# Kernel optimization log

Measured on AMD Instinct MI355X. Metric: run time of the kernel, lower is better.

The kernel has to match this reference:

```python
import jax, jax.numpy as jnp
import numpy as np

N_NODES = 100000
N_EDGES = 1600000
F_IN, F_HID, F_OUT = 128, 256, 128


def setup_inputs() -> dict:
    key = jax.random.key(0)
    ks = jax.random.split(key, 9)
    x = jax.random.normal(ks[0], (N_NODES, F_IN), dtype=jnp.float32)
    edge_src = jax.random.randint(ks[1], (N_EDGES,), 0, N_NODES, dtype=jnp.int32)
    edge_dst = jax.random.randint(ks[2], (N_EDGES,), 0, N_NODES, dtype=jnp.int32)
    s1 = 1.0 / np.sqrt(F_IN)
    s2 = 1.0 / np.sqrt(F_HID)
    W_self1 = jax.random.uniform(ks[3], (F_IN, F_HID), jnp.float32, -s1, s1)
    W_neigh1 = jax.random.uniform(ks[4], (F_IN, F_HID), jnp.float32, -s1, s1)
    b1 = jnp.zeros((F_HID,), jnp.float32)
    W_self2 = jax.random.uniform(ks[5], (F_HID, F_OUT), jnp.float32, -s2, s2)
    W_neigh2 = jax.random.uniform(ks[6], (F_HID, F_OUT), jnp.float32, -s2, s2)
    b2 = jnp.zeros((F_OUT,), jnp.float32)
    return {"x": x, "edge_src": edge_src, "edge_dst": edge_dst,
            "W_self1": W_self1, "W_neigh1": W_neigh1, "b1": b1,
            "W_self2": W_self2, "W_neigh2": W_neigh2, "b2": b2}


def _sage_mean(h, src, dst, W_self, W_neigh, b):
    # mean-aggregate neighbor features onto dst nodes (DGL SAGEConv 'mean')
    deg = jax.ops.segment_sum(jnp.ones_like(src, dtype=h.dtype), dst,
                              num_segments=N_NODES)
    neigh_sum = jax.ops.segment_sum(h[src], dst, num_segments=N_NODES)
    neigh = neigh_sum / jnp.maximum(deg, 1.0)[:, None]
    return h @ W_self + neigh @ W_neigh + b


def reference(x, edge_src, edge_dst, W_self1, W_neigh1, b1, W_self2, W_neigh2, b2):
    h = _sage_mean(x, edge_src, edge_dst, W_self1, W_neigh1, b1)
    h = jax.nn.sigmoid(h)
    h = _sage_mean(h, edge_src, edge_dst, W_self2, W_neigh2, b2)
    return h
```

## Files before the change

### kernel.cpp

```cpp
#include <hip/hip_runtime.h>
#include <hip/hip_bf16.h>

#define N_NODES 100000
#define N_EDGES 1600000
#define F_IN 128
#define F_HID 256
#define F_OUT 128

typedef unsigned short ushort_t;
typedef __attribute__((ext_vector_type(4))) float f32x4;
typedef __attribute__((ext_vector_type(8))) short bf16x8;

#define GAS __attribute__((address_space(1)))
#define LAS __attribute__((address_space(3)))

__device__ __forceinline__ float bf2f(ushort_t u) {
    unsigned int x = ((unsigned int)u) << 16;
    return __builtin_bit_cast(float, x);
}
__device__ __forceinline__ ushort_t f2bf(float f) {
    unsigned int x = __builtin_bit_cast(unsigned int, f);
    unsigned int r = (x + 0x7fffu + ((x >> 16) & 1u)) >> 16;
    return (ushort_t)r;
}

#define NBUCK ((N_NODES + 255) >> 8)
#define CHUNK 4096

__global__ __launch_bounds__(256) void bucket_count_kernel(
    const int* __restrict__ dst, int* __restrict__ bucket_cnt, int n) {
    __shared__ int hist[NBUCK];
    int tid = threadIdx.x;
    int e0 = blockIdx.x * CHUNK;
    int cnt = n - e0; if (cnt > CHUNK) cnt = CHUNK;
    for (int b = tid; b < NBUCK; b += 256) hist[b] = 0;
    __syncthreads();
    for (int i = tid; i < cnt; i += 256) {
        int d = __builtin_nontemporal_load(dst + e0 + i);
        atomicAdd(&hist[d >> 8], 1);
    }
    __syncthreads();
    for (int b = tid; b < NBUCK; b += 256)
        if (hist[b]) atomicAdd(&bucket_cnt[b], hist[b]);
}

__global__ __launch_bounds__(512) void bucket_scan_kernel(
    const int* __restrict__ bucket_cnt, int* __restrict__ bbase,
    int* __restrict__ bcursor, int* __restrict__ rowptr) {
    __shared__ int tmp[512];
    int tid = threadIdx.x;
    int v = (tid < NBUCK) ? bucket_cnt[tid] : 0;
    tmp[tid] = v;
    __syncthreads();
#pragma unroll
    for (int off = 1; off < 512; off <<= 1) {
        int t = (tid >= off) ? tmp[tid - off] : 0;
        __syncthreads();
        tmp[tid] += t;
        __syncthreads();
    }
    if (tid < NBUCK) {
        int base = tmp[tid] - v;
        bbase[tid] = base;
        bcursor[tid] = base;
    }
    if (tid == 0) {
        bbase[NBUCK] = N_EDGES;
        rowptr[N_NODES] = N_EDGES;
    }
}

__global__ __launch_bounds__(256) void bin_edges_kernel(
    const int* __restrict__ src, const int* __restrict__ dst,
    int* __restrict__ bcursor, unsigned int* __restrict__ pairs, int n) {
    __shared__ int sdst[CHUNK];
    __shared__ int ssrc[CHUNK];
    __shared__ int hist[NBUCK];
    __shared__ int resv[NBUCK];
    int tid = threadIdx.x;
    int e0 = blockIdx.x * CHUNK;
    int cnt = n - e0; if (cnt > CHUNK) cnt = CHUNK;
    for (int b = tid; b < NBUCK; b += 256) hist[b] = 0;
    __syncthreads();
    for (int i = tid; i < cnt; i += 256) {
        int d = __builtin_nontemporal_load(dst + e0 + i);
        int s = __builtin_nontemporal_load(src + e0 + i);
        sdst[i] = d;
        ssrc[i] = s;
        atomicAdd(&hist[d >> 8], 1);
    }
    __syncthreads();
    for (int b = tid; b < NBUCK; b += 256) {
        int h = hist[b];
        resv[b] = h ? atomicAdd(&bcursor[b], h) : 0;
        hist[b] = 0;
    }
    __syncthreads();
    for (int i = tid; i < cnt; i += 256) {
        int d = sdst[i], s = ssrc[i];
        int b = d >> 8;
        int off = atomicAdd(&hist[b], 1);
        pairs[resv[b] + off] = ((unsigned)(d & 255) << 17) | (unsigned)s;
    }
}

__global__ __launch_bounds__(256) void sort_bucket_kernel(
    const unsigned int* __restrict__ pairs, const int* __restrict__ bbase,
    int* __restrict__ rowptr, float* __restrict__ invdeg,
    int* __restrict__ csr_src, int nNodes) {
    __shared__ int lcnt[256];
    __shared__ int lrp[256];
    int tid = threadIdx.x;
    int base = blockIdx.x << 8;
    int nn = nNodes - base; if (nn > 256) nn = 256;
    lcnt[tid] = 0;
    __syncthreads();
    int e0 = bbase[blockIdx.x], e1 = bbase[blockIdx.x + 1];
    for (int i = e0 + tid; i < e1; i += 256)
        atomicAdd(&lcnt[pairs[i] >> 17], 1);
    __syncthreads();
    int v = lcnt[tid];
    lrp[tid] = v;
    __syncthreads();
#pragma unroll
    for (int off = 1; off < 256; off <<= 1) {
        int t = (tid >= off) ? lrp[tid - off] : 0;
        __syncthreads();
        lrp[tid] += t;
        __syncthreads();
    }
    lcnt[tid] = 0;
    lrp[tid] = lrp[tid] - v + e0;
    if (tid < nn) {
        rowptr[base + tid] = lrp[tid];
        invdeg[base + tid] = 1.0f / fmaxf((float)v, 1.0f);
    }
    __syncthreads();
    for (int i = e0 + tid; i < e1; i += 256) {
        unsigned pv = pairs[i];
        int j = (int)(pv >> 17);
        int off = atomicAdd(&lcnt[j], 1);
        csr_src[lrp[j] + off] = (int)(pv & 0x1FFFFu);
    }
}

__global__ __launch_bounds__(256) void convert_x_kernel(const float* __restrict__ x,
                                                        ushort_t* __restrict__ A1, int n4) {
    int i = blockIdx.x * 256 + threadIdx.x;
    if (i >= n4) return;
    int e = i * 4;
    int row = e >> 7;
    int col = e & 127;
    f32x4 v = __builtin_nontemporal_load((const f32x4*)(x + (size_t)row * F_IN + col));
    ushort4 o;
    o.x = f2bf(v.x); o.y = f2bf(v.y); o.z = f2bf(v.z); o.w = f2bf(v.w);
    *(ushort4*)(A1 + (size_t)row * 256 + col) = o;
}

__global__ __launch_bounds__(256) void wtransK_kernel(const float* __restrict__ W1,
                                                      const float* __restrict__ W2,
                                                      ushort_t* __restrict__ Wt,
                                                      int Kx, int Ktot, int N) {
    int i = blockIdx.x * 256 + threadIdx.x;
    if (i >= N * Ktot) return;
    int n = i / Ktot, k = i - n * Ktot;
    float v = (k < Kx) ? W1[(size_t)k * N + n] : W2[(size_t)(k - Kx) * N + n];
    Wt[(size_t)n * Ktot + k] = f2bf(v);
}

__global__ __launch_bounds__(256) void wtransN_kernel(const float* __restrict__ Wa,
                                                      const float* __restrict__ Wb,
                                                      ushort_t* __restrict__ Wt,
                                                      int K, int Nh) {
    int i = blockIdx.x * 256 + threadIdx.x;
    if (i >= 2 * Nh * K) return;
    int n = i / K, k = i - n * K;
    const float* W = (n < Nh) ? Wa : Wb;
    int nn = (n < Nh) ? n : n - Nh;
    Wt[(size_t)n * K + k] = f2bf(W[(size_t)k * Nh + nn]);
}

#define ACC8(v)                                                     \
    acc[0] += bf2f((ushort_t)((v).x & 0xffffu));                    \
    acc[1] += bf2f((ushort_t)((v).x >> 16));                        \
    acc[2] += bf2f((ushort_t)((v).y & 0xffffu));                    \
    acc[3] += bf2f((ushort_t)((v).y >> 16));                        \
    acc[4] += bf2f((ushort_t)((v).z & 0xffffu));                    \
    acc[5] += bf2f((ushort_t)((v).z >> 16));                        \
    acc[6] += bf2f((ushort_t)((v).w & 0xffffu));                    \
    acc[7] += bf2f((ushort_t)((v).w >> 16));

template <int MODE>
__global__ __launch_bounds__(256) void gather16_kernel(
    const ushort_t* __restrict__ H, int ldh,
    const int* __restrict__ rowptr, const int* __restrict__ csr_src,
    const float* __restrict__ invdeg,
    const ushort_t* __restrict__ uself, int ldu,
    const float* __restrict__ bias,
    void* __restrict__ outp, int ldo, int nNodes) {
    int lane = threadIdx.x & 63;
    int node = blockIdx.x * 4 + (threadIdx.x >> 6);
    if (node >= nNodes) return;
    int grp = lane >> 4, sub = lane & 15;
    int start = rowptr[node], end = rowptr[node + 1];
    const size_t cofs = (size_t)sub * 8;
    float acc[8] = {};
    for (int e = start + grp; e < end; e += 16) {
        int s0 = csr_src[e];
        uint4 v0 = *(const uint4*)(H + (size_t)s0 * ldh + cofs);
        bool p1 = (e + 4) < end;
        int s1 = p1 ? csr_src[e + 4] : s0;
        uint4 v1 = *(const uint4*)(H + (size_t)s1 * ldh + cofs);
        bool p2 = (e + 8) < end;
        int s2 = p2 ? csr_src[e + 8] : s0;
        uint4 v2 = *(const uint4*)(H + (size_t)s2 * ldh + cofs);
        bool p3 = (e + 12) < end;
        int s3 = p3 ? csr_src[e + 12] : s0;
        uint4 v3 = *(const uint4*)(H + (size_t)s3 * ldh + cofs);
        ACC8(v0);
        if (p1) { ACC8(v1); }
        if (p2) { ACC8(v2); }
        if (p3) { ACC8(v3); }
    }
#pragma unroll
    for (int j = 0; j < 8; ++j) {
        acc[j] += __shfl_xor(acc[j], 16);
        acc[j] += __shfl_xor(acc[j], 32);
    }
    if (grp == 0) {
        float sc = invdeg[node];
        if (MODE == 0) {
            uint4 o;
            o.x = (unsigned)f2bf(acc[0] * sc) | ((unsigned)f2bf(acc[1] * sc) << 16);
            o.y = (unsigned)f2bf(acc[2] * sc) | ((unsigned)f2bf(acc[3] * sc) << 16);
            o.z = (unsigned)f2bf(acc[4] * sc) | ((unsigned)f2bf(acc[5] * sc) << 16);
            o.w = (unsigned)f2bf(acc[6] * sc) | ((unsigned)f2bf(acc[7] * sc) << 16);
            *(uint4*)((ushort_t*)outp + (size_t)node * ldo + cofs) = o;
        } else {
            uint4 us = *(const uint4*)(uself + (size_t)node * ldu + cofs);
            f32x4 o0, o1;
            o0.x = acc[0] * sc + bf2f((ushort_t)(us.x & 0xffffu)) + bias[cofs + 0];
            o0.y = acc[1] * sc + bf2f((ushort_t)(us.x >> 16)) + bias[cofs + 1];
            o0.z = acc[2] * sc + bf2f((ushort_t)(us.y & 0xffffu)) + bias[cofs + 2];
            o0.w = acc[3] * sc + bf2f((ushort_t)(us.y >> 16)) + bias[cofs + 3];
            o1.x = acc[4] * sc + bf2f((ushort_t)(us.z & 0xffffu)) + bias[cofs + 4];
            o1.y = acc[5] * sc + bf2f((ushort_t)(us.z >> 16)) + bias[cofs + 5];
            o1.z = acc[6] * sc + bf2f((ushort_t)(us.w & 0xffffu)) + bias[cofs + 6];
            o1.w = acc[7] * sc + bf2f((ushort_t)(us.w >> 16)) + bias[cofs + 7];
            float* op = (float*)outp + (size_t)node * ldo + cofs;
            __builtin_nontemporal_store(o0, (f32x4*)op);
            __builtin_nontemporal_store(o1, (f32x4*)(op + 4));
        }
    }
}

__global__ __launch_bounds__(256) void gemm_mfma_kernel(
    const ushort_t* __restrict__ A,
    const ushort_t* __restrict__ Bt,
    const float* __restrict__ bias,
    ushort_t* __restrict__ Cout,
    int M, int N, int K, int mode) {
    __shared__ ushort_t shmem[2 * 128 * 64];
    ushort_t* As = shmem;
    ushort_t* Bs = shmem + 128 * 64;
    int tid = threadIdx.x;
    int lane = tid & 63, wid = tid >> 6;
    int l15 = lane & 15, kgrp = lane >> 4, l7 = lane & 7, l8 = lane >> 3;
    int bm = blockIdx.x * 128, bn = blockIdx.y * 128;
    int wr = (wid >> 1) * 64, wc = (wid & 1) * 64;

    f32x4 acc[4][4] = {};

    for (int k0 = 0; k0 < K; k0 += 64) {
#pragma unroll
        for (int t = 0; t < 4; ++t) {
            int c = wid * 4 + t;
            int row = c * 8 + l8;
            int scol = ((l7 ^ (row & 7)) << 3);
            int ar = bm + row; if (ar > M - 1) ar = M - 1;
            __builtin_amdgcn_global_load_lds(
                (const GAS void*)(A + (size_t)ar * K + k0 + scol),
                (LAS void*)(&As[c * 512]), 16, 0, 0);
            int br = bn + row;
            __builtin_amdgcn_global_load_lds(
                (const GAS void*)(Bt + (size_t)br * K + k0 + scol),
                (LAS void*)(&Bs[c * 512]), 16, 0, 0);
        }
        __syncthreads();
#pragma unroll
        for (int kk = 0; kk < 2; ++kk) {
            bf16x8 af[4], bfv[4];
#pragma unroll
            for (int mi = 0; mi < 4; ++mi) {
                int row = wr + mi * 16 + l15;
                int kel = (kk * 32 + kgrp * 8) ^ ((row & 7) << 3);
                af[mi] = *(const bf16x8*)(&As[row * 64 + kel]);
            }
#pragma unroll
            for (int ni = 0; ni < 4; ++ni) {
                int row = wc + ni * 16 + l15;
                int kel = (kk * 32 + kgrp * 8) ^ ((row & 7) << 3);
                bfv[ni] = *(const bf16x8*)(&Bs[row * 64 + kel]);
            }
#pragma unroll
            for (int mi = 0; mi < 4; ++mi)
#pragma unroll
                for (int ni = 0; ni < 4; ++ni)
                    acc[mi][ni] = __builtin_amdgcn_mfma_f32_16x16x32_bf16(
                        af[mi], bfv[ni], acc[mi][ni], 0, 0, 0);
        }
        __syncthreads();
    }

    ushort_t* my = shmem + wid * 4096;
#pragma unroll
    for (int mi = 0; mi < 4; ++mi) {
#pragma unroll
        for (int ni = 0; ni < 4; ++ni) {
            int gcol = bn + wc + ni * 16 + l15;
#pragma unroll
            for (int r = 0; r < 4; ++r) {
                float v = acc[mi][ni][r];
                if (mode == 0) {
                    v += bias[gcol];
                    v = 1.0f / (1.0f + __expf(-v));
                }
                int lr = mi * 16 + kgrp * 4 + r;
                int lc = (ni * 16 + l15) ^ (kgrp << 3);
                my[lr * 64 + lc] = f2bf(v);
            }
        }
    }
#pragma unroll
    for (int it = 0; it < 8; ++it) {
        int r2 = (lane >> 3) + it * 8;
        int c2 = ((lane & 7) << 3) ^ (((r2 >> 2) & 3) << 3);
        bf16x8 vv = *(const bf16x8*)(&my[r2 * 64 + c2]);
        int grow = bm + wr + r2;
        if (grow < M) {
            int gc = bn + wc + (c2 ^ (((r2 >> 2) & 3) << 3));
            *(bf16x8*)(&Cout[(size_t)grow * N + gc]) = vv;
        }
    }
}

extern "C" void kernel_launch(void* const* d_in, const int* in_sizes, int n_in,
                              void* d_out, int out_size, void* d_ws, size_t ws_size,
                              hipStream_t stream) {
    const float* x        = (const float*)d_in[0];
    const int*   src      = (const int*)d_in[1];
    const int*   dst      = (const int*)d_in[2];
    const float* W_self1  = (const float*)d_in[3];
    const float* W_neigh1 = (const float*)d_in[4];
    const float* b1       = (const float*)d_in[5];
    const float* W_self2  = (const float*)d_in[6];
    const float* W_neigh2 = (const float*)d_in[7];
    const float* b2       = (const float*)d_in[8];
    float* out = (float*)d_out;

    char* p = (char*)d_ws;
    auto alloc = [&](size_t bytes) { char* r = p; p += (bytes + 255) & ~(size_t)255; return r; };
    float*    invdeg   = (float*)alloc((size_t)N_NODES * 4);
    ushort_t* A1       = (ushort_t*)alloc((size_t)N_NODES * 256 * 2);
    ushort_t* h        = (ushort_t*)alloc((size_t)N_NODES * 256 * 2);
    ushort_t* u        = (ushort_t*)alloc((size_t)N_NODES * 256 * 2);
    ushort_t* Wt1      = (ushort_t*)alloc((size_t)256 * 256 * 2);
    ushort_t* Wt2      = (ushort_t*)alloc((size_t)256 * 256 * 2);
    int* rowptr        = (int*)alloc((size_t)(N_NODES + 1) * 4);
    int* bucket_cnt    = (int*)alloc((size_t)NBUCK * 4);
    int* bbase         = (int*)alloc((size_t)(NBUCK + 1) * 4);
    int* bcursor       = (int*)alloc((size_t)NBUCK * 4);
    unsigned int* pairs= (unsigned int*)alloc((size_t)N_EDGES * 4);
    int* csr_src       = (int*)alloc((size_t)N_EDGES * 4);

    convert_x_kernel<<<(N_NODES * F_IN / 4 + 255) / 256, 256, 0, stream>>>(
        x, A1, N_NODES * F_IN / 4);
    wtransK_kernel<<<(256 * 256 + 255) / 256, 256, 0, stream>>>(
        W_self1, W_neigh1, Wt1, 128, 256, 256);
    wtransN_kernel<<<(256 * 256 + 255) / 256, 256, 0, stream>>>(
        W_self2, W_neigh2, Wt2, 256, 128);

    hipMemsetAsync(bucket_cnt, 0, (size_t)NBUCK * sizeof(int), stream);
    bucket_count_kernel<<<(N_EDGES + CHUNK - 1) / CHUNK, 256, 0, stream>>>(
        dst, bucket_cnt, N_EDGES);
    bucket_scan_kernel<<<1, 512, 0, stream>>>(bucket_cnt, bbase, bcursor, rowptr);
    bin_edges_kernel<<<(N_EDGES + CHUNK - 1) / CHUNK, 256, 0, stream>>>(
        src, dst, bcursor, pairs, N_EDGES);
    sort_bucket_kernel<<<NBUCK, 256, 0, stream>>>(
        pairs, bbase, rowptr, invdeg, csr_src, N_NODES);

    gather16_kernel<0><<<(N_NODES + 3) / 4, 256, 0, stream>>>(
        A1, 256, rowptr, csr_src, invdeg, nullptr, 0, nullptr, A1 + 128, 256, N_NODES);
    {
        dim3 grid((N_NODES + 127) / 128, 2);
        gemm_mfma_kernel<<<grid, 256, 0, stream>>>(A1, Wt1, b1, h, N_NODES, 256, 256, 0);
    }

    {
        dim3 grid((N_NODES + 127) / 128, 2);
        gemm_mfma_kernel<<<grid, 256, 0, stream>>>(h, Wt2, nullptr, u, N_NODES, 256, 256, 1);
    }
    gather16_kernel<1><<<(N_NODES + 3) / 4, 256, 0, stream>>>(
        u + 128, 256, rowptr, csr_src, invdeg, u, 256, b2, out, 128, N_NODES);
}
```

Measured before the change: 308.3 us.

## Split feature buffers into compact 128-wide arrays and gather two nodes per wave

The interleaved 256-wide A1 and u buffers become separate compact 128-column arrays (xb/agg, uself/uneigh). The gathered rows are therefore dense 256-byte rows, which should improve cache-line and L2 locality for the random neighbour reads. The GEMM now reads its K dimension from two source pointers and splits its output columns across two destinations. The gather is also rewritten as a persistent grid-stride kernel where each wave processes two nodes at once, issuing eight independent row loads per iteration to raise memory-level parallelism, at the cost of more registers and some wasted predicated loads.

```diff
diff --git a/kernel.cpp b/kernel.cpp
--- a/kernel.cpp
+++ b/kernel.cpp
@@ -145,16 +145,14 @@
 }
 
 __global__ __launch_bounds__(256) void convert_x_kernel(const float* __restrict__ x,
-                                                        ushort_t* __restrict__ A1, int n4) {
+                                                        ushort_t* __restrict__ xb, int n4) {
     int i = blockIdx.x * 256 + threadIdx.x;
     if (i >= n4) return;
     int e = i * 4;
-    int row = e >> 7;
-    int col = e & 127;
-    f32x4 v = __builtin_nontemporal_load((const f32x4*)(x + (size_t)row * F_IN + col));
+    f32x4 v = __builtin_nontemporal_load((const f32x4*)(x + e));
     ushort4 o;
     o.x = f2bf(v.x); o.y = f2bf(v.y); o.z = f2bf(v.z); o.w = f2bf(v.w);
-    *(ushort4*)(A1 + (size_t)row * 256 + col) = o;
+    *(ushort4*)(xb + e) = o;
 }
 
 __global__ __launch_bounds__(256) void wtransK_kernel(const float* __restrict__ W1,
@@ -180,86 +178,147 @@
     Wt[(size_t)n * K + k] = f2bf(W[(size_t)k * Nh + nn]);
 }
 
-#define ACC8(v)                                                     \
-    acc[0] += bf2f((ushort_t)((v).x & 0xffffu));                    \
-    acc[1] += bf2f((ushort_t)((v).x >> 16));                        \
-    acc[2] += bf2f((ushort_t)((v).y & 0xffffu));                    \
-    acc[3] += bf2f((ushort_t)((v).y >> 16));                        \
-    acc[4] += bf2f((ushort_t)((v).z & 0xffffu));                    \
-    acc[5] += bf2f((ushort_t)((v).z >> 16));                        \
-    acc[6] += bf2f((ushort_t)((v).w & 0xffffu));                    \
-    acc[7] += bf2f((ushort_t)((v).w >> 16));
+#define ACC8(arr, v)                                                \
+    arr[0] += bf2f((ushort_t)((v).x & 0xffffu));                    \
+    arr[1] += bf2f((ushort_t)((v).x >> 16));                        \
+    arr[2] += bf2f((ushort_t)((v).y & 0xffffu));                    \
+    arr[3] += bf2f((ushort_t)((v).y >> 16));                        \
+    arr[4] += bf2f((ushort_t)((v).z & 0xffffu));                    \
+    arr[5] += bf2f((ushort_t)((v).z >> 16));                        \
+    arr[6] += bf2f((ushort_t)((v).w & 0xffffu));                    \
+    arr[7] += bf2f((ushort_t)((v).w >> 16));
 
 template <int MODE>
-__global__ __launch_bounds__(256) void gather16_kernel(
-    const ushort_t* __restrict__ H, int ldh,
-    const int* __restrict__ rowptr, const int* __restrict__ csr_src,
+__global__ __launch_bounds__(256) void gather2_kernel(
+    const ushort_t* __restrict__ H,
+    const int* __restrict__ rowptr,
+    const int* __restrict__ csr_src,
     const float* __restrict__ invdeg,
-    const ushort_t* __restrict__ uself, int ldu,
+    const ushort_t* __restrict__ uself,
     const float* __restrict__ bias,
-    void* __restrict__ outp, int ldo, int nNodes) {
+    void* __restrict__ outp,
+    int nNodes, int totWaves) {
     int lane = threadIdx.x & 63;
-    int node = blockIdx.x * 4 + (threadIdx.x >> 6);
-    if (node >= nNodes) return;
+    int wv = blockIdx.x * 4 + (threadIdx.x >> 6);
     int grp = lane >> 4, sub = lane & 15;
-    int start = rowptr[node], end = rowptr[node + 1];
     const size_t cofs = (size_t)sub * 8;
-    float acc[8] = {};
-    for (int e = start + grp; e < end; e += 16) {
-        int s0 = csr_src[e];
-        uint4 v0 = *(const uint4*)(H + (size_t)s0 * ldh + cofs);
-        bool p1 = (e + 4) < end;
-        int s1 = p1 ? csr_src[e + 4] : s0;
-        uint4 v1 = *(const uint4*)(H + (size_t)s1 * ldh + cofs);
-        bool p2 = (e + 8) < end;
-        int s2 = p2 ? csr_src[e + 8] : s0;
-        uint4 v2 = *(const uint4*)(H + (size_t)s2 * ldh + cofs);
-        bool p3 = (e + 12) < end;
-        int s3 = p3 ? csr_src[e + 12] : s0;
-        uint4 v3 = *(const uint4*)(H + (size_t)s3 * ldh + cofs);
-        ACC8(v0);
-        if (p1) { ACC8(v1); }
-        if (p2) { ACC8(v2); }
-        if (p3) { ACC8(v3); }
-    }
-#pragma unroll
-    for (int j = 0; j < 8; ++j) {
-        acc[j] += __shfl_xor(acc[j], 16);
-        acc[j] += __shfl_xor(acc[j], 32);
-    }
-    if (grp == 0) {
-        float sc = invdeg[node];
-        if (MODE == 0) {
-            uint4 o;
-            o.x = (unsigned)f2bf(acc[0] * sc) | ((unsigned)f2bf(acc[1] * sc) << 16);
-            o.y = (unsigned)f2bf(acc[2] * sc) | ((unsigned)f2bf(acc[3] * sc) << 16);
-            o.z = (unsigned)f2bf(acc[4] * sc) | ((unsigned)f2bf(acc[5] * sc) << 16);
-            o.w = (unsigned)f2bf(acc[6] * sc) | ((unsigned)f2bf(acc[7] * sc) << 16);
-            *(uint4*)((ushort_t*)outp + (size_t)node * ldo + cofs) = o;
-        } else {
-            uint4 us = *(const uint4*)(uself + (size_t)node * ldu + cofs);
-            f32x4 o0, o1;
-            o0.x = acc[0] * sc + bf2f((ushort_t)(us.x & 0xffffu)) + bias[cofs + 0];
-            o0.y = acc[1] * sc + bf2f((ushort_t)(us.x >> 16)) + bias[cofs + 1];
-            o0.z = acc[2] * sc + bf2f((ushort_t)(us.y & 0xffffu)) + bias[cofs + 2];
-            o0.w = acc[3] * sc + bf2f((ushort_t)(us.y >> 16)) + bias[cofs + 3];
-            o1.x = acc[4] * sc + bf2f((ushort_t)(us.z & 0xffffu)) + bias[cofs + 4];
-            o1.y = acc[5] * sc + bf2f((ushort_t)(us.z >> 16)) + bias[cofs + 5];
-            o1.z = acc[6] * sc + bf2f((ushort_t)(us.w & 0xffffu)) + bias[cofs + 6];
-            o1.w = acc[7] * sc + bf2f((ushort_t)(us.w >> 16)) + bias[cofs + 7];
-            float* op = (float*)outp + (size_t)node * ldo + cofs;
-            __builtin_nontemporal_store(o0, (f32x4*)op);
-            __builtin_nontemporal_store(o1, (f32x4*)(op + 4));
-        }
+    int pair = wv;
+    if (pair * 2 >= nNodes) return;
+    int r0 = rowptr[pair * 2];
+    int r1 = rowptr[pair * 2 + 1];
+    int r2 = rowptr[pair * 2 + 2];
+    while (true) {
+        int npair = pair + totWaves;
+        bool hasNext = (npair * 2 < nNodes);
+        int n0 = 0, n1 = 0, n2 = 0;
+        if (hasNext) {
+            n0 = rowptr[npair * 2];
+            n1 = rowptr[npair * 2 + 1];
+            n2 = rowptr[npair * 2 + 2];
+        }
+        int nodeA = pair * 2;
+        int sA = r0, eA = r1, sB = r1, eB = r2;
+        int cA = sA < N_EDGES ? sA : N_EDGES - 1;
+        int cB = sB < N_EDGES ? sB : N_EDGES - 1;
+        float accA[8] = {}, accB[8] = {};
+        for (int ea = sA + grp, eb = sB + grp; ea < eA || eb < eB; ea += 16, eb += 16) {
+            bool pa0 = ea < eA, pa1 = ea + 4 < eA, pa2 = ea + 8 < eA, pa3 = ea + 12 < eA;
+            bool pb0 = eb < eB, pb1 = eb + 4 < eB, pb2 = eb + 8 < eB, pb3 = eb + 12 < eB;
+            int ja0 = pa0 ? ea : cA, ja1 = pa1 ? ea + 4 : cA;
+            int ja2 = pa2 ? ea + 8 : cA, ja3 = pa3 ? ea + 12 : cA;
+            int jb0 = pb0 ? eb : cB, jb1 = pb1 ? eb + 4 : cB;
+            int jb2 = pb2 ? eb + 8 : cB, jb3 = pb3 ? eb + 12 : cB;
+            int sa0 = csr_src[ja0], sa1 = csr_src[ja1];
+            int sa2 = csr_src[ja2], sa3 = csr_src[ja3];
+            int sb0 = csr_src[jb0], sb1 = csr_src[jb1];
+            int sb2 = csr_src[jb2], sb3 = csr_src[jb3];
+            uint4 va0 = *(const uint4*)(H + (size_t)sa0 * 128 + cofs);
+            uint4 va1 = *(const uint4*)(H + (size_t)sa1 * 128 + cofs);
+            uint4 va2 = *(const uint4*)(H + (size_t)sa2 * 128 + cofs);
+            uint4 va3 = *(const uint4*)(H + (size_t)sa3 * 128 + cofs);
+            uint4 vb0 = *(const uint4*)(H + (size_t)sb0 * 128 + cofs);
+            uint4 vb1 = *(const uint4*)(H + (size_t)sb1 * 128 + cofs);
+            uint4 vb2 = *(const uint4*)(H + (size_t)sb2 * 128 + cofs);
+            uint4 vb3 = *(const uint4*)(H + (size_t)sb3 * 128 + cofs);
+            if (pa0) { ACC8(accA, va0); }
+            if (pa1) { ACC8(accA, va1); }
+            if (pa2) { ACC8(accA, va2); }
+            if (pa3) { ACC8(accA, va3); }
+            if (pb0) { ACC8(accB, vb0); }
+            if (pb1) { ACC8(accB, vb1); }
+            if (pb2) { ACC8(accB, vb2); }
+            if (pb3) { ACC8(accB, vb3); }
+        }
+#pragma unroll
+        for (int j = 0; j < 8; ++j) {
+            accA[j] += __shfl_xor(accA[j], 16);
+            accA[j] += __shfl_xor(accA[j], 32);
+            accB[j] += __shfl_xor(accB[j], 16);
+            accB[j] += __shfl_xor(accB[j], 32);
+        }
+        if (grp == 0) {
+            int nodeB = nodeA + 1;
+            float scA = invdeg[nodeA];
+            float scB = (nodeB < nNodes) ? invdeg[nodeB] : 1.0f;
+            if (MODE == 0) {
+                uint4 o;
+                o.x = (unsigned)f2bf(accA[0] * scA) | ((unsigned)f2bf(accA[1] * scA) << 16);
+                o.y = (unsigned)f2bf(accA[2] * scA) | ((unsigned)f2bf(accA[3] * scA) << 16);
+                o.z = (unsigned)f2bf(accA[4] * scA) | ((unsigned)f2bf(accA[5] * scA) << 16);
+                o.w = (unsigned)f2bf(accA[6] * scA) | ((unsigned)f2bf(accA[7] * scA) << 16);
+                *(uint4*)((ushort_t*)outp + (size_t)nodeA * 128 + cofs) = o;
+                if (nodeB < nNodes) {
+                    uint4 p2;
+                    p2.x = (unsigned)f2bf(accB[0] * scB) | ((unsigned)f2bf(accB[1] * scB) << 16);
+                    p2.y = (unsigned)f2bf(accB[2] * scB) | ((unsigned)f2bf(accB[3] * scB) << 16);
+                    p2.z = (unsigned)f2bf(accB[4] * scB) | ((unsigned)f2bf(accB[5] * scB) << 16);
+                    p2.w = (unsigned)f2bf(accB[6] * scB) | ((unsigned)f2bf(accB[7] * scB) << 16);
+                    *(uint4*)((ushort_t*)outp + (size_t)nodeB * 128 + cofs) = p2;
+                }
+            } else {
+                uint4 us = *(const uint4*)(uself + (size_t)nodeA * 128 + cofs);
+                f32x4 o0, o1;
+                o0.x = accA[0] * scA + bf2f((ushort_t)(us.x & 0xffffu)) + bias[cofs + 0];
+                o0.y = accA[1] * scA + bf2f((ushort_t)(us.x >> 16)) + bias[cofs + 1];
+                o0.z = accA[2] * scA + bf2f((ushort_t)(us.y & 0xffffu)) + bias[cofs + 2];
+                o0.w = accA[3] * scA + bf2f((ushort_t)(us.y >> 16)) + bias[cofs + 3];
+                o1.x = accA[4] * scA + bf2f((ushort_t)(us.z & 0xffffu)) + bias[cofs + 4];
+                o1.y = accA[5] * scA + bf2f((ushort_t)(us.z >> 16)) + bias[cofs + 5];
+                o1.z = accA[6] * scA + bf2f((ushort_t)(us.w & 0xffffu)) + bias[cofs + 6];
+                o1.w = accA[7] * scA + bf2f((ushort_t)(us.w >> 16)) + bias[cofs + 7];
+                float* op = (float*)outp + (size_t)nodeA * 128 + cofs;
+                __builtin_nontemporal_store(o0, (f32x4*)op);
+                __builtin_nontemporal_store(o1, (f32x4*)(op + 4));
+                if (nodeB < nNodes) {
+                    uint4 u2 = *(const uint4*)(uself + (size_t)nodeB * 128 + cofs);
+                    f32x4 q0, q1;
+                    q0.x = accB[0] * scB + bf2f((ushort_t)(u2.x & 0xffffu)) + bias[cofs + 0];
+                    q0.y = accB[1] * scB + bf2f((ushort_t)(u2.x >> 16)) + bias[cofs + 1];
+                    q0.z = accB[2] * scB + bf2f((ushort_t)(u2.y & 0xffffu)) + bias[cofs + 2];
+                    q0.w = accB[3] * scB + bf2f((ushort_t)(u2.y >> 16)) + bias[cofs + 3];
+                    q1.x = accB[4] * scB + bf2f((ushort_t)(u2.z & 0xffffu)) + bias[cofs + 4];
+                    q1.y = accB[5] * scB + bf2f((ushort_t)(u2.z >> 16)) + bias[cofs + 5];
+                    q1.z = accB[6] * scB + bf2f((ushort_t)(u2.w & 0xffffu)) + bias[cofs + 6];
+                    q1.w = accB[7] * scB + bf2f((ushort_t)(u2.w >> 16)) + bias[cofs + 7];
+                    float* oq = (float*)outp + (size_t)nodeB * 128 + cofs;
+                    __builtin_nontemporal_store(q0, (f32x4*)oq);
+                    __builtin_nontemporal_store(q1, (f32x4*)(oq + 4));
+                }
+            }
+        }
+        if (!hasNext) break;
+        pair = npair; r0 = n0; r1 = n1; r2 = n2;
     }
 }
 
 __global__ __launch_bounds__(256) void gemm_mfma_kernel(
-    const ushort_t* __restrict__ A,
+    const ushort_t* __restrict__ A1, int lda1,
+    const ushort_t* __restrict__ A2, int lda2, int Kx,
     const ushort_t* __restrict__ Bt,
     const float* __restrict__ bias,
-    ushort_t* __restrict__ Cout,
-    int M, int N, int K, int mode) {
+    ushort_t* __restrict__ CoutA, int ldcA,
+    ushort_t* __restrict__ CoutB, int ldcB,
+    int M, int mode) {
     __shared__ ushort_t shmem[2 * 128 * 64];
     ushort_t* As = shmem;
     ushort_t* Bs = shmem + 128 * 64;
@@ -271,7 +330,10 @@
 
     f32x4 acc[4][4] = {};
 
-    for (int k0 = 0; k0 < K; k0 += 64) {
+    for (int k0 = 0; k0 < 256; k0 += 64) {
+        const ushort_t* Ap = (k0 < Kx) ? A1 : A2;
+        int lda = (k0 < Kx) ? lda1 : lda2;
+        int kk0 = (k0 < Kx) ? k0 : k0 - Kx;
 #pragma unroll
         for (int t = 0; t < 4; ++t) {
             int c = wid * 4 + t;
@@ -279,11 +341,11 @@
             int scol = ((l7 ^ (row & 7)) << 3);
             int ar = bm + row; if (ar > M - 1) ar = M - 1;
             __builtin_amdgcn_global_load_lds(
-                (const GAS void*)(A + (size_t)ar * K + k0 + scol),
+                (const GAS void*)(Ap + (size_t)ar * lda + kk0 + scol),
                 (LAS void*)(&As[c * 512]), 16, 0, 0);
             int br = bn + row;
             __builtin_amdgcn_global_load_lds(
-                (const GAS void*)(Bt + (size_t)br * K + k0 + scol),
+                (const GAS void*)(Bt + (size_t)br * 256 + k0 + scol),
                 (LAS void*)(&Bs[c * 512]), 16, 0, 0);
         }
         __syncthreads();
@@ -334,12 +396,16 @@
 #pragma unroll
     for (int it = 0; it < 8; ++it) {
         int r2 = (lane >> 3) + it * 8;
-        int c2 = ((lane & 7) << 3) ^ (((r2 >> 2) & 3) << 3);
+        int swz = ((r2 >> 2) & 3) << 3;
+        int c2 = ((lane & 7) << 3) ^ swz;
         bf16x8 vv = *(const bf16x8*)(&my[r2 * 64 + c2]);
         int grow = bm + wr + r2;
         if (grow < M) {
-            int gc = bn + wc + (c2 ^ (((r2 >> 2) & 3) << 3));
-            *(bf16x8*)(&Cout[(size_t)grow * N + gc]) = vv;
+            int gc = bn + wc + (c2 ^ swz);
+            ushort_t* dstp = (gc < 128)
+                ? CoutA + (size_t)grow * ldcA + gc
+                : CoutB + (size_t)grow * ldcB + (gc - 128);
+            *(bf16x8*)dstp = vv;
         }
     }
 }
@@ -361,9 +427,11 @@
     char* p = (char*)d_ws;
     auto alloc = [&](size_t bytes) { char* r = p; p += (bytes + 255) & ~(size_t)255; return r; };
     float*    invdeg   = (float*)alloc((size_t)N_NODES * 4);
-    ushort_t* A1       = (ushort_t*)alloc((size_t)N_NODES * 256 * 2);
+    ushort_t* xb       = (ushort_t*)alloc((size_t)N_NODES * 128 * 2);
+    ushort_t* agg      = (ushort_t*)alloc((size_t)N_NODES * 128 * 2);
     ushort_t* h        = (ushort_t*)alloc((size_t)N_NODES * 256 * 2);
-    ushort_t* u        = (ushort_t*)alloc((size_t)N_NODES * 256 * 2);
+    ushort_t* uself    = (ushort_t*)alloc((size_t)N_NODES * 128 * 2);
+    ushort_t* uneigh   = (ushort_t*)alloc((size_t)N_NODES * 128 * 2);
     ushort_t* Wt1      = (ushort_t*)alloc((size_t)256 * 256 * 2);
     ushort_t* Wt2      = (ushort_t*)alloc((size_t)256 * 256 * 2);
     int* rowptr        = (int*)alloc((size_t)(N_NODES + 1) * 4);
@@ -374,7 +442,7 @@
     int* csr_src       = (int*)alloc((size_t)N_EDGES * 4);
 
     convert_x_kernel<<<(N_NODES * F_IN / 4 + 255) / 256, 256, 0, stream>>>(
-        x, A1, N_NODES * F_IN / 4);
+        x, xb, N_NODES * F_IN / 4);
     wtransK_kernel<<<(256 * 256 + 255) / 256, 256, 0, stream>>>(
         W_self1, W_neigh1, Wt1, 128, 256, 256);
     wtransN_kernel<<<(256 * 256 + 255) / 256, 256, 0, stream>>>(
@@ -389,17 +457,22 @@
     sort_bucket_kernel<<<NBUCK, 256, 0, stream>>>(
         pairs, bbase, rowptr, invdeg, csr_src, N_NODES);
 
-    gather16_kernel<0><<<(N_NODES + 3) / 4, 256, 0, stream>>>(
-        A1, 256, rowptr, csr_src, invdeg, nullptr, 0, nullptr, A1 + 128, 256, N_NODES);
+    const int GATHER_BLOCKS = 2048;
+    const int TOT_WAVES = GATHER_BLOCKS * 4;
+
+    gather2_kernel<0><<<GATHER_BLOCKS, 256, 0, stream>>>(
+        xb, rowptr, csr_src, invdeg, nullptr, nullptr, agg, N_NODES, TOT_WAVES);
     {
         dim3 grid((N_NODES + 127) / 128, 2);
-        gemm_mfma_kernel<<<grid, 256, 0, stream>>>(A1, Wt1, b1, h, N_NODES, 256, 256, 0);
+        gemm_mfma_kernel<<<grid, 256, 0, stream>>>(
+            xb, 128, agg, 128, 128, Wt1, b1, h, 256, h + 128, 256, N_NODES, 0);
     }
 
     {
         dim3 grid((N_NODES + 127) / 128, 2);
-        gemm_mfma_kernel<<<grid, 256, 0, stream>>>(h, Wt2, nullptr, u, N_NODES, 256, 256, 1);
-    }
-    gather16_kernel<1><<<(N_NODES + 3) / 4, 256, 0, stream>>>(
-        u + 128, 256, rowptr, csr_src, invdeg, u, 256, b2, out, 128, N_NODES);
-}
+        gemm_mfma_kernel<<<grid, 256, 0, stream>>>(
+            h, 256, h, 256, 256, Wt2, nullptr, uself, 128, uneigh, 128, N_NODES, 1);
+    }
+    gather2_kernel<1><<<GATHER_BLOCKS, 256, 0, stream>>>(
+        uneigh, rowptr, csr_src, invdeg, uself, b2, out, N_NODES, TOT_WAVES);
+}
```

Result: faster. 292.5 us (-5.1%).
